# Performance work log

Measured on AMD Instinct MI355X. Metric: run time of the kernel, lower is better.

The kernel has to match this reference:

```python
import jax, jax.numpy as jnp
import numpy as np

B, S, D, H = 4, 2048, 1024, 16
DH = D // H


def setup_inputs() -> dict:
    key = jax.random.key(0)
    ks = jax.random.split(key, 5)
    scale = 0.02
    return {
        "in_features": jax.random.normal(ks[0], (B, S, D), dtype=jnp.float32),
        "Wq": jax.random.normal(ks[1], (D, D), dtype=jnp.float32) * scale,
        "Wk": jax.random.normal(ks[2], (D, D), dtype=jnp.float32) * scale,
        "Wv": jax.random.normal(ks[3], (D, D), dtype=jnp.float32) * scale,
        "Wo": jax.random.normal(ks[4], (D, D), dtype=jnp.float32) * scale,
    }


def reference(in_features, Wq, Wk, Wv, Wo):
    x = in_features  # [B, S, D]
    # projections: einsum '... s d_in, d_model d_in -> ... s d_model'  == x @ W.T
    q = jnp.einsum('bsd,md->bsm', x, Wq)
    k = jnp.einsum('bsd,md->bsm', x, Wk)
    v = jnp.einsum('bsd,md->bsm', x, Wv)
    # split heads: [B, H, S, DH]
    q = q.reshape(B, S, H, DH).transpose(0, 2, 1, 3)
    k = k.reshape(B, S, H, DH).transpose(0, 2, 1, 3)
    v = v.reshape(B, S, H, DH).transpose(0, 2, 1, 3)
    scale = 1.0 / jnp.sqrt(jnp.asarray(DH, dtype=q.dtype))
    scores = jnp.einsum('bhqd,bhkd->bhqk', q, k) * scale  # [B, H, S, S]
    causal = jnp.tril(jnp.ones((S, S), dtype=bool))
    scores = jnp.where(causal[None, None, :, :], scores, -jnp.inf)
    attn = jax.nn.softmax(scores, axis=-1)
    out = jnp.einsum('bhqk,bhkd->bhqd', attn, v)  # [B, H, S, DH]
    out = out.transpose(0, 2, 1, 3).reshape(B, S, D)
    # output projection: einsum '... s d_v, d_model d_v -> ... s d_model' == out @ Wo.T
    return jnp.einsum('bsd,md->bsm', out, Wo)
```

## Files before the change

kernel.cpp:

```cpp
#include <hip/hip_runtime.h>

typedef unsigned short u16;
typedef unsigned int u32;
typedef __attribute__((ext_vector_type(8))) short bf16x8;
typedef __attribute__((ext_vector_type(4))) short bf16x4;
typedef __attribute__((ext_vector_type(4))) float f32x4;

#define S_LEN 2048
#define NHEAD 16
#define DHEAD 64
#define DMODEL 1024

__device__ __forceinline__ u16 f2bf(float f) {
  unsigned u = __builtin_bit_cast(unsigned, f);
  unsigned r = (u + 0x7fffu + ((u >> 16) & 1u)) >> 16;
  return (u16)r;
}

__device__ __forceinline__ void gld_lds16(const void* g, void* l) {
  __builtin_amdgcn_global_load_lds((const __attribute__((address_space(1))) unsigned*)g,
                                   (__attribute__((address_space(3))) unsigned*)l,
                                   16, 0, 0);
}

__global__ void cast_bf16_kernel(const float* __restrict__ in, u16* __restrict__ out, int n4) {
  int i = blockIdx.x * 256 + threadIdx.x;
  if (i >= n4) return;
  float4 v = reinterpret_cast<const float4*>(in)[i];
  ushort4 o;
  o.x = f2bf(v.x); o.y = f2bf(v.y); o.z = f2bf(v.z); o.w = f2bf(v.w);
  reinterpret_cast<ushort4*>(out)[i] = o;
}

__global__ void cast_w_kernel(const float* __restrict__ Wq, const float* __restrict__ Wk,
                              const float* __restrict__ Wv, const float* __restrict__ Wo,
                              u16* __restrict__ out) {
  int id = blockIdx.x * 256 + threadIdx.x;
  int wsel = id >> 18, j = id & 262143;
  const float* s = wsel < 2 ? (wsel == 0 ? Wq : Wk) : (wsel == 2 ? Wv : Wo);
  float4 v = reinterpret_cast<const float4*>(s)[j];
  ushort4 o;
  o.x = f2bf(v.x); o.y = f2bf(v.y); o.z = f2bf(v.z); o.w = f2bf(v.w);
  reinterpret_cast<ushort4*>(out)[id] = o;
}

#define MFMA_Q(mlo, nlo)                                                                     \
  _Pragma("unroll") for (int m_ = 0; m_ < 4; ++m_)                                           \
  _Pragma("unroll") for (int n_ = 0; n_ < 2; ++n_)                                           \
  _Pragma("unroll") for (int kk_ = 0; kk_ < 2; ++kk_)                                        \
    acc[(mlo) + m_][(nlo) + n_] = __builtin_amdgcn_mfma_f32_16x16x32_bf16(                   \
        af[(mlo) + m_][kk_], bf[(nlo) + n_][kk_], acc[(mlo) + m_][(nlo) + n_], 0, 0, 0);

#define VM6 do { __builtin_amdgcn_sched_barrier(0);                                          \
  asm volatile("s_waitcnt vmcnt(6)" ::: "memory");                                           \
  __builtin_amdgcn_sched_barrier(0); } while (0)
#define VM0 do { __builtin_amdgcn_sched_barrier(0);                                          \
  asm volatile("s_waitcnt vmcnt(0)" ::: "memory");                                           \
  __builtin_amdgcn_sched_barrier(0); } while (0)

#define HALF_ITER(bb, S1, S2, S3, S4, WAIT) do {                                             \
  const u16* aB = aB0 + (bb)*32768;                                                          \
  const u16* bB = bB0 + (bb)*32768;                                                          \
                                                                                     \
  _Pragma("unroll") for (int m_ = 0; m_ < 4; ++m_) {                                         \
    af[m_][0] = rdA(aB, m_, 0); af[m_][1] = rdA(aB, m_, 1); }                                \
  _Pragma("unroll") for (int n_ = 0; n_ < 2; ++n_) {                                         \
    bf[n_][0] = rdB(bB, n_, 0); bf[n_][1] = rdB(bB, n_, 1); }                                \
  S1;                                                                                        \
  __builtin_amdgcn_s_barrier();                                                              \
  __builtin_amdgcn_s_setprio(1); MFMA_Q(0, 0) __builtin_amdgcn_s_setprio(0);                 \
  __builtin_amdgcn_s_barrier();                                                              \
                                                                                     \
  _Pragma("unroll") for (int m_ = 0; m_ < 4; ++m_) {                                         \
    af[4 + m_][0] = rdA(aB, 4 + m_, 0); af[4 + m_][1] = rdA(aB, 4 + m_, 1); }                \
  S2;                                                                                        \
  __builtin_amdgcn_s_barrier();                                                              \
  __builtin_amdgcn_s_setprio(1); MFMA_Q(4, 0) __builtin_amdgcn_s_setprio(0);                 \
  __builtin_amdgcn_s_barrier();                                                              \
                                                                                     \
  _Pragma("unroll") for (int n_ = 0; n_ < 2; ++n_) {                                         \
    bf[2 + n_][0] = rdB(bB, 2 + n_, 0); bf[2 + n_][1] = rdB(bB, 2 + n_, 1); }                \
  S3;                                                                                        \
  __builtin_amdgcn_s_barrier();                                                              \
  __builtin_amdgcn_s_setprio(1); MFMA_Q(0, 2) __builtin_amdgcn_s_setprio(0);                 \
  __builtin_amdgcn_s_barrier();                                                              \
                                                                                     \
  S4;                                                                                        \
  __builtin_amdgcn_s_barrier();                                                              \
  __builtin_amdgcn_s_setprio(1); MFMA_Q(4, 2) __builtin_amdgcn_s_setprio(0);                 \
  WAIT;                                                                                      \
  __builtin_amdgcn_s_barrier();                                                              \
} while (0)

__global__ __launch_bounds__(512, 2) void gemm_qkv(const u16* __restrict__ A,
                                                   const u16* __restrict__ Bw,
                                                   u16* __restrict__ Qb) {
  __shared__ u16 lds[65536];
  const int bid = blockIdx.x;
  const int xcd = bid & 7, v = bid >> 3;
  const int by = xcd * 4 + (v & 3), bx = v >> 2;
  const int brow = by * 256, bcol = bx * 256;
  const int tid = threadIdx.x;
  const int w = tid >> 6, lane = tid & 63;
  const int wm = w >> 2, wn = w & 3;
  const int c = lane & 15, qr = lane >> 4;
  const int sqz = (qr ^ (c & 7)) * 8;

  auto stg = [&](int mat, int tau, int half) {
    if (tau >= 16) return;
    u16* region = lds + (tau & 1) * 32768 + mat * 16384 + half * 8192;
    const u16* G = mat ? Bw : A;
    int rowb = (mat ? bcol : brow) + half * 128;
    int k0 = tau * 64;
#pragma unroll
    for (int i = 0; i < 2; ++i) {
      int slot = i * 512 + tid;
      int r = slot >> 3, cb = slot & 7;
      int cbs = cb ^ (r & 7);
      gld_lds16(G + (size_t)(rowb + r) * DMODEL + k0 + cbs * 8, region + (i * 512 + w * 64) * 8);
    }
  };

  auto rdA = [&](const u16* base, int m, int kk) {
    return *(const bf16x8*)(base + (m * 16 + c) * 64 + (sqz ^ (kk << 5)));
  };
  auto rdB = [&](const u16* base, int n, int kk) {
    return *(const bf16x8*)(base + ((wn & 1) * 64 + n * 16 + c) * 64 + (sqz ^ (kk << 5)));
  };

  f32x4 acc[8][4];
#pragma unroll
  for (int m = 0; m < 8; ++m)
#pragma unroll
    for (int n = 0; n < 4; ++n) acc[m][n] = (f32x4){0.f, 0.f, 0.f, 0.f};
  bf16x8 af[8][2], bf[4][2];
  const u16* aB0 = lds + wm * 8192;
  const u16* bB0 = lds + 16384 + (wn >> 1) * 8192;

  stg(0, 0, 0); stg(0, 0, 1); stg(1, 0, 0); stg(1, 0, 1);
  stg(0, 1, 0); stg(0, 1, 1); stg(1, 1, 0);
  VM6;
  __builtin_amdgcn_s_barrier();

#pragma unroll 1
  for (int t = 0; t < 8; ++t) {
    const int e = 2 * t;
    HALF_ITER(0,
              stg(1, e + 1, 1),
              stg(0, e + 2, 0),
              stg(0, e + 2, 1),
              stg(1, e + 2, 0),
              if (t < 7) { VM6; } else { VM0; });
    HALF_ITER(1,
              stg(1, e + 2, 1),
              stg(0, e + 3, 0),
              stg(0, e + 3, 1),
              stg(1, e + 3, 0),
              if (t < 7) { VM6; });
  }

  u16* Kb = Qb + 8388608;
  u16* Vt = Kb + 8388608;
#pragma unroll
  for (int m = 0; m < 8; ++m) {
#pragma unroll
    for (int n = 0; n < 4; ++n) {
      f32x4 a = acc[m][n];
      int gm0 = brow + wm * 128 + m * 16 + qr * 4;
      int gn = bcol + wn * 64 + n * 16 + c;
      int mat = gn >> 10, gl = gn & 1023;
      int hh = gl >> 6, dh = gl & 63;
      int b = gm0 >> 11;
      if (mat == 2) {
        int s0 = gm0 & 2047;
        ushort4 pk;
        pk.x = f2bf(a[0]); pk.y = f2bf(a[1]); pk.z = f2bf(a[2]); pk.w = f2bf(a[3]);
        *reinterpret_cast<ushort4*>(Vt + ((size_t)(b * NHEAD + hh) * DHEAD + dh) * S_LEN + s0) = pk;
      } else {
        float scale = (mat == 0) ? 0.1803368801111204f : 1.0f;
        u16* dst = (mat == 0) ? Qb : Kb;
#pragma unroll
        for (int r = 0; r < 4; ++r) {
          int gm = gm0 + r;
          int s = gm & 2047;
          dst[((size_t)(b * NHEAD + hh) * S_LEN + s) * DHEAD + dh] = f2bf(a[r] * scale);
        }
      }
    }
  }
}

__global__ __launch_bounds__(256) void gemm_bt(const u16* __restrict__ A, const u16* __restrict__ Bw,
                                               float* __restrict__ outp) {
  __shared__ u16 lA[2][128 * 32];
  __shared__ u16 lB[2][128 * 32];
  const int hw = blockIdx.x;
  const int xcd = hw & 7, vv = hw >> 3;
  const int bx = vv >> 3, by = xcd * 8 + (vv & 7);
  const int tid = threadIdx.x;
  const int w = tid >> 6, lane = tid & 63;
  const int wm = w >> 1, wn = w & 1;
  const int c = lane & 15, qr = lane >> 4;
  const int brow = by * 128, bcol = bx * 128;
  f32x4 acc[4][4];
#pragma unroll
  for (int m = 0; m < 4; ++m)
#pragma unroll
    for (int n = 0; n < 4; ++n) acc[m][n] = (f32x4){0.f, 0.f, 0.f, 0.f};

  auto stage = [&](int kt, int bsel) {
    const int k0 = kt * 32;
#pragma unroll
    for (int i = 0; i < 2; ++i) {
      int slot = i * 256 + w * 64 + lane;
      int r = slot >> 2, sg = slot & 3;
      gld_lds16(A + (size_t)(brow + r) * DMODEL + k0 + sg * 8, &lA[bsel][(i * 256 + w * 64) * 8]);
      gld_lds16(Bw + (size_t)(bcol + r) * DMODEL + k0 + sg * 8, &lB[bsel][(i * 256 + w * 64) * 8]);
    }
  };

  stage(0, 0);
  __syncthreads();
  int cur = 0;
  for (int kt = 0; kt < 32; ++kt) {
    if (kt < 31) stage(kt + 1, cur ^ 1);
    bf16x8 af[4], bfr[4];
#pragma unroll
    for (int m = 0; m < 4; ++m) af[m] = *(const bf16x8*)(&lA[cur][(wm * 64 + m * 16 + c) * 32 + qr * 8]);
#pragma unroll
    for (int n = 0; n < 4; ++n) bfr[n] = *(const bf16x8*)(&lB[cur][(wn * 64 + n * 16 + c) * 32 + qr * 8]);
    __builtin_amdgcn_s_setprio(1);
#pragma unroll
    for (int m = 0; m < 4; ++m)
#pragma unroll
      for (int n = 0; n < 4; ++n)
        acc[m][n] = __builtin_amdgcn_mfma_f32_16x16x32_bf16(af[m], bfr[n], acc[m][n], 0, 0, 0);
    __builtin_amdgcn_s_setprio(0);
    __syncthreads();
    cur ^= 1;
  }

  const int rb = qr * 4;
#pragma unroll
  for (int m = 0; m < 4; ++m)
#pragma unroll
    for (int n = 0; n < 4; ++n) {
      f32x4 a = acc[m][n];
      int gm0 = brow + wm * 64 + m * 16 + rb;
      int gn = bcol + wn * 64 + n * 16 + c;
#pragma unroll
      for (int r = 0; r < 4; ++r) outp[(size_t)(gm0 + r) * DMODEL + gn] = a[r];
    }
}

__global__ __launch_bounds__(512, 4) void attn_kernel(const u16* __restrict__ Q, const u16* __restrict__ K,
                                                      const u16* __restrict__ Vt, u16* __restrict__ O) {
  __shared__ u16 lsK[2][64 * 64];
  __shared__ u16 lsV[2][64 * 64];
  __shared__ u16 lsP[8][16 * 64];
  const int hw = blockIdx.x;
  const int xcd = hw & 7, vv = hw >> 3;
  const int by = xcd * 8 + (vv >> 3);
  const int j = vv & 7;
  const int tid = threadIdx.x;
  const int w = tid >> 6, lane = tid & 63;
  const int c = lane & 15, qr = lane >> 4;
  const int b = by >> 4, h = by & 15;
  u16* lp = lsP[w];

  const int q0A = j * 128 + w * 16;
  const int q0B = (15 - j) * 128 + w * 16;
  const int ndA = q0A >> 6, ndB = q0B >> 6;
  const int ntiles = 32 - 2 * j;

  const u16* qra = Q + ((size_t)by * S_LEN + q0A + c) * DHEAD;
  const u16* qrb = Q + ((size_t)by * S_LEN + q0B + c) * DHEAD;
  const bf16x8 aQA0 = *(const bf16x8*)(qra + qr * 8);
  const bf16x8 aQA1 = *(const bf16x8*)(qra + 32 + qr * 8);
  const bf16x8 aQB0 = *(const bf16x8*)(qrb + qr * 8);
  const bf16x8 aQB1 = *(const bf16x8*)(qrb + 32 + qr * 8);

  f32x4 oA[4], oB[4];
#pragma unroll
  for (int d = 0; d < 4; ++d) { oA[d] = (f32x4){0.f, 0.f, 0.f, 0.f}; oB[d] = oA[d]; }
  float mA = -1e30f, lA_ = 0.f, mB = -1e30f, lB_ = 0.f;

  auto stage = [&](int kt, int bsel) {
    const int kv0 = kt * 64;
    int r = tid >> 3, p = tid & 7;
    int ps = p ^ (r & 7);
    gld_lds16(K + ((size_t)by * S_LEN + kv0 + r) * DHEAD + ps * 8, &lsK[bsel][(w * 64) * 8]);
    gld_lds16(Vt + ((size_t)by * DHEAD + r) * S_LEN + kv0 + ps * 8, &lsV[bsel][(w * 64) * 8]);
  };

  auto process = [&](const u16* bK, const u16* bV, int kt, int nd, int q0,
                     const bf16x8& aQ0, const bf16x8& aQ1,
                     f32x4* o_acc, float& m_run, float& l_run) {
    const int kv0 = kt * 64;
    f32x4 sc[4];
    __builtin_amdgcn_s_setprio(1);
#pragma unroll
    for (int nt = 0; nt < 4; ++nt) {
      int row = nt * 16 + c;
      const bf16x8 k0 = *(const bf16x8*)(bK + row * 64 + ((qr ^ (row & 7)) * 8));
      const bf16x8 k1 = *(const bf16x8*)(bK + row * 64 + (((4 + qr) ^ (row & 7)) * 8));
      f32x4 z = (f32x4){0.f, 0.f, 0.f, 0.f};
      z = __builtin_amdgcn_mfma_f32_16x16x32_bf16(k0, aQ0, z, 0, 0, 0);
      z = __builtin_amdgcn_mfma_f32_16x16x32_bf16(k1, aQ1, z, 0, 0, 0);
      sc[nt] = z;
    }
    __builtin_amdgcn_s_setprio(0);

    if (kt == nd) {
#pragma unroll
      for (int nt = 0; nt < 4; ++nt)
#pragma unroll
        for (int r = 0; r < 4; ++r) {
          int k_g = kv0 + nt * 16 + qr * 4 + r;
          int q_g = q0 + c;
          if (k_g > q_g) sc[nt][r] = -1e30f;
        }
    }

    float tm = fmaxf(fmaxf(fmaxf(sc[0][0], sc[0][1]), fmaxf(sc[0][2], sc[0][3])),
                     fmaxf(fmaxf(sc[1][0], sc[1][1]), fmaxf(sc[1][2], sc[1][3])));
    tm = fmaxf(tm, fmaxf(fmaxf(fmaxf(sc[2][0], sc[2][1]), fmaxf(sc[2][2], sc[2][3])),
                         fmaxf(fmaxf(sc[3][0], sc[3][1]), fmaxf(sc[3][2], sc[3][3]))));
    tm = fmaxf(tm, __shfl_xor(tm, 16));
    tm = fmaxf(tm, __shfl_xor(tm, 32));
    if (tm > m_run + 11.5f) {
      float al = __builtin_amdgcn_exp2f(m_run - tm);
      l_run *= al;
#pragma unroll
      for (int dt = 0; dt < 4; ++dt)
#pragma unroll
        for (int r = 0; r < 4; ++r) o_acc[dt][r] *= al;
      m_run = tm;
    }
    float rs = 0.f;
#pragma unroll
    for (int nt = 0; nt < 4; ++nt) {
      float p0 = __builtin_amdgcn_exp2f(sc[nt][0] - m_run);
      float p1 = __builtin_amdgcn_exp2f(sc[nt][1] - m_run);
      float p2 = __builtin_amdgcn_exp2f(sc[nt][2] - m_run);
      float p3 = __builtin_amdgcn_exp2f(sc[nt][3] - m_run);
      rs += (p0 + p1) + (p2 + p3);
      u32 w01 = __builtin_amdgcn_perm(__builtin_bit_cast(u32, p1), __builtin_bit_cast(u32, p0), 0x07060302u);
      u32 w23 = __builtin_amdgcn_perm(__builtin_bit_cast(u32, p3), __builtin_bit_cast(u32, p2), 0x07060302u);
      uint2 pk; pk.x = w01; pk.y = w23;
      *reinterpret_cast<uint2*>(lp + c * 64 + (((nt * 4 + qr) ^ c) * 4)) = pk;
    }
    rs += __shfl_xor(rs, 16);
    rs += __shfl_xor(rs, 32);
    l_run += rs;

    bf16x8 pb[2];
#pragma unroll
    for (int ks = 0; ks < 2; ++ks) {
      bf16x4 lo = *(const bf16x4*)(lp + c * 64 + (((ks * 8 + qr * 2) ^ c) * 4));
      bf16x4 hi = *(const bf16x4*)(lp + c * 64 + (((ks * 8 + qr * 2 + 1) ^ c) * 4));
      pb[ks] = (bf16x8){lo[0], lo[1], lo[2], lo[3], hi[0], hi[1], hi[2], hi[3]};
    }
    __builtin_amdgcn_s_setprio(1);
#pragma unroll
    for (int dt = 0; dt < 4; ++dt) {
      int rowv = dt * 16 + c;
#pragma unroll
      for (int ks = 0; ks < 2; ++ks) {
        const bf16x8 vb = *(const bf16x8*)(bV + rowv * 64 + (((ks * 4 + qr) ^ (rowv & 7)) * 8));
        o_acc[dt] = __builtin_amdgcn_mfma_f32_16x16x32_bf16(vb, pb[ks], o_acc[dt], 0, 0, 0);
      }
    }
    __builtin_amdgcn_s_setprio(0);
  };

  stage(0, 0);
  __syncthreads();
  for (int kt = 0; kt < ntiles; kt += 2) {
    if (kt + 1 < ntiles) stage(kt + 1, 1);
    if (kt <= ndB) process(lsK[0], lsV[0], kt, ndB, q0B, aQB0, aQB1, oB, mB, lB_);
    if (kt <= ndA) process(lsK[0], lsV[0], kt, ndA, q0A, aQA0, aQA1, oA, mA, lA_);
    __syncthreads();
    const int k2 = kt + 1;
    if (k2 + 1 < ntiles) stage(k2 + 1, 0);
    if (k2 <= ndB) process(lsK[1], lsV[1], k2, ndB, q0B, aQB0, aQB1, oB, mB, lB_);
    if (k2 <= ndA) process(lsK[1], lsV[1], k2, ndA, q0A, aQA0, aQA1, oA, mA, lA_);
    __syncthreads();
  }

  {
    float rl = 1.0f / lB_;
    int s = q0B + c;
#pragma unroll
    for (int dt = 0; dt < 4; ++dt) {
      ushort4 ok;
#pragma unroll
      for (int r = 0; r < 4; ++r) ((u16*)&ok)[r] = f2bf(oB[dt][r] * rl);
      *reinterpret_cast<ushort4*>(O + (((size_t)b * S_LEN + s) * NHEAD + h) * DHEAD + dt * 16 + qr * 4) = ok;
    }
  }
  {
    float rl = 1.0f / lA_;
    int s = q0A + c;
#pragma unroll
    for (int dt = 0; dt < 4; ++dt) {
      ushort4 ok;
#pragma unroll
      for (int r = 0; r < 4; ++r) ((u16*)&ok)[r] = f2bf(oA[dt][r] * rl);
      *reinterpret_cast<ushort4*>(O + (((size_t)b * S_LEN + s) * NHEAD + h) * DHEAD + dt * 16 + qr * 4) = ok;
    }
  }
}

extern "C" void kernel_launch(void* const* d_in, const int* in_sizes, int n_in,
                              void* d_out, int out_size, void* d_ws, size_t ws_size,
                              hipStream_t stream) {
  (void)in_sizes; (void)n_in; (void)out_size; (void)ws_size;
  const float* x  = (const float*)d_in[0];
  const float* Wq = (const float*)d_in[1];
  const float* Wk = (const float*)d_in[2];
  const float* Wv = (const float*)d_in[3];
  const float* Wo = (const float*)d_in[4];

  u16* ws  = (u16*)d_ws;
  u16* xb  = ws;
  u16* wqb = xb  + 8388608;
  u16* wob = wqb + 3145728;
  u16* Qb  = wqb + 4194304;
  u16* Kb  = Qb  + 8388608;
  u16* Vt  = Kb  + 8388608;
  u16* Ob  = Vt  + 8388608;

  cast_bf16_kernel<<<8192, 256, 0, stream>>>(x, xb, 2097152);
  cast_w_kernel<<<4096, 256, 0, stream>>>(Wq, Wk, Wv, Wo, wqb);

  gemm_qkv<<<384, 512, 0, stream>>>(xb, wqb, Qb);
  attn_kernel<<<512, 512, 0, stream>>>(Qb, Kb, Vt, Ob);
  gemm_bt<<<512, 256, 0, stream>>>(Ob, wob, (float*)d_out);
}
```

Baseline: 178.4 us.

## Retile QKV GEMM to 256x192 blocks with 4x2 warp grid and 512 blocks

Changes the fused QKV projection GEMM tile from 256x256 to 256x192 and rearranges the 8 warps into a 4x2 grid, so each warp computes 64x96. The grid grows from 384 to 512 blocks, which should fill the GPU's compute units more evenly and reduce tail imbalance. LDS per block drops, and the staging schedule and vmcnt waits are reworked to fit the new tile. In exchange, each block reuses less data per tile and sends more loads to global memory relative to its compute.

```diff
diff --git a/kernel.cpp b/kernel.cpp
--- a/kernel.cpp
+++ b/kernel.cpp
@@ -45,49 +45,48 @@
 }
 
 #define MFMA_Q(mlo, nlo)                                                                     \
-  _Pragma("unroll") for (int m_ = 0; m_ < 4; ++m_)                                           \
-  _Pragma("unroll") for (int n_ = 0; n_ < 2; ++n_)                                           \
+  _Pragma("unroll") for (int m_ = 0; m_ < 2; ++m_)                                           \
+  _Pragma("unroll") for (int n_ = 0; n_ < 3; ++n_)                                           \
   _Pragma("unroll") for (int kk_ = 0; kk_ < 2; ++kk_)                                        \
     acc[(mlo) + m_][(nlo) + n_] = __builtin_amdgcn_mfma_f32_16x16x32_bf16(                   \
         af[(mlo) + m_][kk_], bf[(nlo) + n_][kk_], acc[(mlo) + m_][(nlo) + n_], 0, 0, 0);
 
-#define VM6 do { __builtin_amdgcn_sched_barrier(0);                                          \
-  asm volatile("s_waitcnt vmcnt(6)" ::: "memory");                                           \
+#define VM5 do { __builtin_amdgcn_sched_barrier(0);                                          \
+  asm volatile("s_waitcnt vmcnt(5)" ::: "memory");                                           \
   __builtin_amdgcn_sched_barrier(0); } while (0)
 #define VM0 do { __builtin_amdgcn_sched_barrier(0);                                          \
   asm volatile("s_waitcnt vmcnt(0)" ::: "memory");                                           \
   __builtin_amdgcn_sched_barrier(0); } while (0)
 
-#define HALF_ITER(bb, S1, S2, S3, S4, WAIT) do {                                             \
-  const u16* aB = aB0 + (bb)*32768;                                                          \
-  const u16* bB = bB0 + (bb)*32768;                                                          \
-                                                                                     \
-  _Pragma("unroll") for (int m_ = 0; m_ < 4; ++m_) {                                         \
-    af[m_][0] = rdA(aB, m_, 0); af[m_][1] = rdA(aB, m_, 1); }                                \
-  _Pragma("unroll") for (int n_ = 0; n_ < 2; ++n_) {                                         \
-    bf[n_][0] = rdB(bB, n_, 0); bf[n_][1] = rdB(bB, n_, 1); }                                \
-  S1;                                                                                        \
+#define HALF_ITER(bb, e, WAIT) do {                                                          \
+  const u16* aW = aW0 + (bb)*28672;                                                          \
+  const u16* bW = bW0 + (bb)*28672;                                                          \
+                              \
+  _Pragma("unroll") for (int m_ = 0; m_ < 2; ++m_) {                                         \
+    af[m_][0] = rdA(aW, m_, 0); af[m_][1] = rdA(aW, m_, 1); }                                \
+  _Pragma("unroll") for (int n_ = 0; n_ < 3; ++n_) {                                         \
+    bf[n_][0] = rdB(bW, n_, 0); bf[n_][1] = rdB(bW, n_, 1); }                                \
+  stgB((e) + 1, 1); stgB((e) + 1, 2);                                                        \
   __builtin_amdgcn_s_barrier();                                                              \
   __builtin_amdgcn_s_setprio(1); MFMA_Q(0, 0) __builtin_amdgcn_s_setprio(0);                 \
   __builtin_amdgcn_s_barrier();                                                              \
-                                                                                     \
-  _Pragma("unroll") for (int m_ = 0; m_ < 4; ++m_) {                                         \
-    af[4 + m_][0] = rdA(aB, 4 + m_, 0); af[4 + m_][1] = rdA(aB, 4 + m_, 1); }                \
-  S2;                                                                                        \
-  __builtin_amdgcn_s_barrier();                                                              \
-  __builtin_amdgcn_s_setprio(1); MFMA_Q(4, 0) __builtin_amdgcn_s_setprio(0);                 \
-  __builtin_amdgcn_s_barrier();                                                              \
-                                                                                     \
-  _Pragma("unroll") for (int n_ = 0; n_ < 2; ++n_) {                                         \
-    bf[2 + n_][0] = rdB(bB, 2 + n_, 0); bf[2 + n_][1] = rdB(bB, 2 + n_, 1); }                \
-  S3;                                                                                        \
-  __builtin_amdgcn_s_barrier();                                                              \
-  __builtin_amdgcn_s_setprio(1); MFMA_Q(0, 2) __builtin_amdgcn_s_setprio(0);                 \
-  __builtin_amdgcn_s_barrier();                                                              \
-                                                                                     \
-  S4;                                                                                        \
-  __builtin_amdgcn_s_barrier();                                                              \
-  __builtin_amdgcn_s_setprio(1); MFMA_Q(4, 2) __builtin_amdgcn_s_setprio(0);                 \
+                                                                       \
+  _Pragma("unroll") for (int m_ = 0; m_ < 2; ++m_) {                                         \
+    af[2 + m_][0] = rdA(aW, 2 + m_, 0); af[2 + m_][1] = rdA(aW, 2 + m_, 1); }                \
+  __builtin_amdgcn_s_barrier();                                                              \
+  __builtin_amdgcn_s_setprio(1); MFMA_Q(2, 0) __builtin_amdgcn_s_setprio(0);                 \
+  __builtin_amdgcn_s_barrier();                                                              \
+                         \
+  _Pragma("unroll") for (int n_ = 0; n_ < 3; ++n_) {                                         \
+    bf[3 + n_][0] = rdB(bW, 3 + n_, 0); bf[3 + n_][1] = rdB(bW, 3 + n_, 1); }                \
+  stgA((e) + 2, 0); stgA((e) + 2, 1);                                                        \
+  __builtin_amdgcn_s_barrier();                                                              \
+  __builtin_amdgcn_s_setprio(1); MFMA_Q(0, 3) __builtin_amdgcn_s_setprio(0);                 \
+  __builtin_amdgcn_s_barrier();                                                              \
+                                          \
+  stgB((e) + 2, 0);                                                                          \
+  __builtin_amdgcn_s_barrier();                                                              \
+  __builtin_amdgcn_s_setprio(1); MFMA_Q(2, 3) __builtin_amdgcn_s_setprio(0);                 \
   WAIT;                                                                                      \
   __builtin_amdgcn_s_barrier();                                                              \
 } while (0)
@@ -95,79 +94,77 @@
 __global__ __launch_bounds__(512, 2) void gemm_qkv(const u16* __restrict__ A,
                                                    const u16* __restrict__ Bw,
                                                    u16* __restrict__ Qb) {
-  __shared__ u16 lds[65536];
+  __shared__ u16 lds[57344];
   const int bid = blockIdx.x;
   const int xcd = bid & 7, v = bid >> 3;
   const int by = xcd * 4 + (v & 3), bx = v >> 2;
-  const int brow = by * 256, bcol = bx * 256;
+  const int brow = by * 256, bcol = bx * 192;
   const int tid = threadIdx.x;
   const int w = tid >> 6, lane = tid & 63;
-  const int wm = w >> 2, wn = w & 3;
+  const int wm = w >> 1, wn = w & 1;
   const int c = lane & 15, qr = lane >> 4;
   const int sqz = (qr ^ (c & 7)) * 8;
 
-  auto stg = [&](int mat, int tau, int half) {
+  auto stgA = [&](int tau, int half) {
     if (tau >= 16) return;
-    u16* region = lds + (tau & 1) * 32768 + mat * 16384 + half * 8192;
-    const u16* G = mat ? Bw : A;
-    int rowb = (mat ? bcol : brow) + half * 128;
+    u16* region = lds + (tau & 1) * 28672 + half * 8192;
+    int rowb = brow + half * 128;
     int k0 = tau * 64;
 #pragma unroll
     for (int i = 0; i < 2; ++i) {
       int slot = i * 512 + tid;
       int r = slot >> 3, cb = slot & 7;
       int cbs = cb ^ (r & 7);
-      gld_lds16(G + (size_t)(rowb + r) * DMODEL + k0 + cbs * 8, region + (i * 512 + w * 64) * 8);
-    }
+      gld_lds16(A + (size_t)(rowb + r) * DMODEL + k0 + cbs * 8, region + (i * 512 + w * 64) * 8);
+    }
+  };
+  auto stgB = [&](int tau, int third) {
+    if (tau >= 16) return;
+    u16* region = lds + (tau & 1) * 28672 + 16384 + third * 4096;
+    int rowb = bcol + third * 64;
+    int k0 = tau * 64;
+    int r = tid >> 3, cb = tid & 7;
+    int cbs = cb ^ (r & 7);
+    gld_lds16(Bw + (size_t)(rowb + r) * DMODEL + k0 + cbs * 8, region + (w * 64) * 8);
   };
 
   auto rdA = [&](const u16* base, int m, int kk) {
     return *(const bf16x8*)(base + (m * 16 + c) * 64 + (sqz ^ (kk << 5)));
   };
   auto rdB = [&](const u16* base, int n, int kk) {
-    return *(const bf16x8*)(base + ((wn & 1) * 64 + n * 16 + c) * 64 + (sqz ^ (kk << 5)));
-  };
-
-  f32x4 acc[8][4];
-#pragma unroll
-  for (int m = 0; m < 8; ++m)
-#pragma unroll
-    for (int n = 0; n < 4; ++n) acc[m][n] = (f32x4){0.f, 0.f, 0.f, 0.f};
-  bf16x8 af[8][2], bf[4][2];
-  const u16* aB0 = lds + wm * 8192;
-  const u16* bB0 = lds + 16384 + (wn >> 1) * 8192;
-
-  stg(0, 0, 0); stg(0, 0, 1); stg(1, 0, 0); stg(1, 0, 1);
-  stg(0, 1, 0); stg(0, 1, 1); stg(1, 1, 0);
-  VM6;
+    return *(const bf16x8*)(base + (n * 16 + c) * 64 + (sqz ^ (kk << 5)));
+  };
+
+  f32x4 acc[4][6];
+#pragma unroll
+  for (int m = 0; m < 4; ++m)
+#pragma unroll
+    for (int n = 0; n < 6; ++n) acc[m][n] = (f32x4){0.f, 0.f, 0.f, 0.f};
+  bf16x8 af[4][2], bf[6][2];
+  const u16* aW0 = lds + wm * 4096;
+  const u16* bW0 = lds + 16384 + wn * 6144;
+
+  stgA(0, 0); stgA(0, 1); stgB(0, 0); stgB(0, 1); stgB(0, 2);
+  stgA(1, 0); stgA(1, 1); stgB(1, 0);
+  VM5;
   __builtin_amdgcn_s_barrier();
 
 #pragma unroll 1
   for (int t = 0; t < 8; ++t) {
     const int e = 2 * t;
-    HALF_ITER(0,
-              stg(1, e + 1, 1),
-              stg(0, e + 2, 0),
-              stg(0, e + 2, 1),
-              stg(1, e + 2, 0),
-              if (t < 7) { VM6; } else { VM0; });
-    HALF_ITER(1,
-              stg(1, e + 2, 1),
-              stg(0, e + 3, 0),
-              stg(0, e + 3, 1),
-              stg(1, e + 3, 0),
-              if (t < 7) { VM6; });
+    HALF_ITER(0, e, if (t < 7) { VM5; } else { VM0; });
+    HALF_ITER(1, e + 1, if (t < 7) { VM5; });
   }
 
   u16* Kb = Qb + 8388608;
   u16* Vt = Kb + 8388608;
 #pragma unroll
-  for (int m = 0; m < 8; ++m) {
-#pragma unroll
-    for (int n = 0; n < 4; ++n) {
+  for (int m = 0; m < 4; ++m) {
+#pragma unroll
+    for (int n = 0; n < 6; ++n) {
       f32x4 a = acc[m][n];
-      int gm0 = brow + wm * 128 + m * 16 + qr * 4;
-      int gn = bcol + wn * 64 + n * 16 + c;
+      int gm0 = brow + wm * 64 + m * 16 + qr * 4;
+      int gn = bcol + wn * 96 + n * 16 + c;
       int mat = gn >> 10, gl = gn & 1023;
       int hh = gl >> 6, dh = gl & 63;
       int b = gm0 >> 11;
@@ -434,7 +431,7 @@
   cast_bf16_kernel<<<8192, 256, 0, stream>>>(x, xb, 2097152);
   cast_w_kernel<<<4096, 256, 0, stream>>>(Wq, Wk, Wv, Wo, wqb);
 
-  gemm_qkv<<<384, 512, 0, stream>>>(xb, wqb, Qb);
+  gemm_qkv<<<512, 512, 0, stream>>>(xb, wqb, Qb);
   attn_kernel<<<512, 512, 0, stream>>>(Qb, Kb, Vt, Ob);
   gemm_bt<<<512, 256, 0, stream>>>(Ob, wob, (float*)d_out);
 }
```

Result: faster. 173.8 us (-2.6%).
